# Kernel tuning notes

Measured on AMD Instinct MI355X. Metric: run time of the kernel, lower is better.

Reference implementation:

```python
import jax, jax.numpy as jnp
import numpy as np

D_MODEL = 1024
HEADS = 16
SEQ = 2048
BATCH = 4
NEG_INF = -1e9
LN_EPS = 1e-5


def setup_inputs() -> dict:
    key = jax.random.key(0)
    ks = jax.random.split(key, 10)
    B, S, D = BATCH, SEQ, D_MODEL
    # xavier_uniform bound for square D x D linear
    bound = np.sqrt(6.0 / (D + D))
    def xavier(k):
        return jax.random.uniform(k, (D, D), jnp.float32, -bound, bound)
    return {
        "q": jax.random.normal(ks[0], (B, S, D), jnp.float32),
        "k": jax.random.normal(ks[1], (B, S, D), jnp.float32),
        "v": jax.random.normal(ks[2], (B, S, D), jnp.float32),
        "Wq": xavier(ks[3]),
        "Wk": xavier(ks[4]),
        "Wv": xavier(ks[5]),
        "Wo": xavier(ks[6]),
        "ln_gamma": jnp.ones((D,), jnp.float32),
        "ln_beta": jnp.zeros((D,), jnp.float32),
        "sen_len": jax.random.randint(ks[7], (B,), 1, S + 1, jnp.int32),
    }


def reference(q, k, v, Wq, Wk, Wv, Wo, ln_gamma, ln_beta, sen_len):
    B, S, D = q.shape
    H = HEADS
    d = D // H
    residual = q
    # projections (Linear with weight W applies x @ W.T)
    qh = jnp.einsum('bsd,ed->bse', q, Wq).reshape(B, S, H, d).transpose(0, 2, 1, 3)
    kh = jnp.einsum('bsd,ed->bse', k, Wk).reshape(B, S, H, d).transpose(0, 2, 1, 3)
    vh = jnp.einsum('bsd,ed->bse', v, Wv).reshape(B, S, H, d).transpose(0, 2, 1, 3)
    # scores [B,H,S,S]
    scores = jnp.einsum('bhqd,bhkd->bhqk', qh, kh) / np.sqrt(d).astype(np.float32)
    # padding mask on keys: j >= sen_len[b]; causal mask: j > i
    pad = jnp.arange(S)[None, :] >= sen_len[:, None]          # [B, S]
    causal = jnp.triu(jnp.ones((S, S), bool), 1)               # [S, S]
    mask = pad[:, None, None, :] | causal[None, None, :, :]
    scores = jnp.where(mask, NEG_INF, scores)
    att = jax.nn.softmax(scores, axis=-1)
    ctx = jnp.einsum('bhqk,bhkd->bhqd', att, vh)               # [B,H,S,d]
    ctx = ctx.transpose(0, 2, 1, 3).reshape(B, S, D)
    out = jnp.einsum('bsd,ed->bse', ctx, Wo)
    out = out + residual
    mean = out.mean(-1, keepdims=True)
    var = out.var(-1, keepdims=True)
    out = (out - mean) * jax.lax.rsqrt(var + LN_EPS) * ln_gamma + ln_beta
    return out
```

## Files before the change

### kernel.cpp

```cpp
#include <hip/hip_runtime.h>

typedef __bf16 bf16;
typedef bf16 bf16x8 __attribute__((ext_vector_type(8)));
typedef bf16 bf16x4 __attribute__((ext_vector_type(4)));
typedef float f32x4 __attribute__((ext_vector_type(4)));

#define ASYNC16(gp, lp) __builtin_amdgcn_global_load_lds( \
    (__attribute__((address_space(1))) void*)(const void*)(gp), \
    (__attribute__((address_space(3))) void*)(lp), 16, 0, 0)

__device__ __forceinline__ bf16x8 cvt2(const float4 a, const float4 b) {
    bf16x8 t;
    t[0] = (bf16)a.x; t[1] = (bf16)a.y; t[2] = (bf16)a.z; t[3] = (bf16)a.w;
    t[4] = (bf16)b.x; t[5] = (bf16)b.y; t[6] = (bf16)b.z; t[7] = (bf16)b.w;
    return t;
}

__global__ __launch_bounds__(256)
void cvt_w3(const float* __restrict__ W0, const float* __restrict__ W1,
            const float* __restrict__ W2, bf16* __restrict__ out)
{
    const int z = blockIdx.y;
    const float* src = (z == 0) ? W0 : (z == 1) ? W1 : W2;
    const int i = blockIdx.x * 256 + threadIdx.x;
    const float4 a = ((const float4*)src)[i * 2];
    const float4 b = ((const float4*)src)[i * 2 + 1];
    *(bf16x8*)&out[((size_t)z << 20) + (size_t)i * 8] = cvt2(a, b);
}

__global__ __launch_bounds__(256)
void cvt_w1(const float* __restrict__ W, bf16* __restrict__ out)
{
    const int i = blockIdx.x * 256 + threadIdx.x;
    const float4 a = ((const float4*)W)[i * 2];
    const float4 b = ((const float4*)W)[i * 2 + 1];
    *(bf16x8*)&out[(size_t)i * 8] = cvt2(a, b);
}

__global__ __launch_bounds__(256, 2)
void proj_gemm(const float* __restrict__ Aq, const float* __restrict__ Ak,
               const float* __restrict__ Av, const bf16* __restrict__ Wb3,
               bf16* __restrict__ Qp, bf16* __restrict__ Kp, bf16* __restrict__ Vt)
{
    constexpr int K = 1024;
    constexpr int BK = 32;
    __shared__ __align__(16) bf16 As[128 * BK];
    __shared__ __align__(16) bf16 Bs[128 * BK];

    const int z = blockIdx.z;
    const float* A = (z == 0) ? Aq : (z == 1) ? Ak : Av;
    const bf16* W = Wb3 + ((size_t)z << 20);

    const int tid  = threadIdx.x;
    const int lane = tid & 63;
    const int w    = tid >> 6;
    const int wr   = w >> 1, wc = w & 1;
    const int m0   = blockIdx.y * 128;
    const int n0   = blockIdx.x * 128;

    f32x4 acc[4][4] = {};

    for (int k0 = 0; k0 < K; k0 += BK) {
        #pragma unroll
        for (int i = 0; i < 2; ++i) {
            const int c   = w * 128 + i * 64 + lane;
            const int row = c >> 2, kg = c & 3;
            ASYNC16(W + (size_t)(n0 + row) * K + k0 + kg * 8, &Bs[c * 8]);
            const float* ap = A + (size_t)(m0 + row) * K + k0 + kg * 8;
            *(bf16x8*)&As[c * 8] = cvt2(*(const float4*)ap, *(const float4*)(ap + 4));
        }
        __syncthreads();
        bf16x8 af[4], bfr[4];
        #pragma unroll
        for (int t = 0; t < 4; ++t) {
            af[t]  = *(const bf16x8*)&As[(wr * 64 + t * 16 + (lane & 15)) * BK + (lane >> 4) * 8];
            bfr[t] = *(const bf16x8*)&Bs[(wc * 64 + t * 16 + (lane & 15)) * BK + (lane >> 4) * 8];
        }
        #pragma unroll
        for (int mt = 0; mt < 4; ++mt)
            #pragma unroll
            for (int nt = 0; nt < 4; ++nt)
                acc[mt][nt] = __builtin_amdgcn_mfma_f32_16x16x32_bf16(af[mt], bfr[nt], acc[mt][nt], 0, 0, 0);
        __syncthreads();
    }

    #pragma unroll
    for (int mt = 0; mt < 4; ++mt) {
        #pragma unroll
        for (int nt = 0; nt < 4; ++nt) {
            const int mbase = m0 + wr * 64 + mt * 16 + ((lane >> 4) << 2);
            const int n     = n0 + wc * 64 + nt * 16 + (lane & 15);
            const int h = n >> 6, dd = n & 63;
            if (z < 2) {
                bf16* out = (z == 0) ? Qp : Kp;
                #pragma unroll
                for (int r = 0; r < 4; ++r) {
                    const int m = mbase + r;
                    const int b = m >> 11, s = m & 2047;
                    out[(((size_t)(b * 16 + h)) * 2048 + s) * 64 + dd] = (bf16)acc[mt][nt][r];
                }
            } else {
                const int b = mbase >> 11, s = mbase & 2047;
                bf16x4 v4;
                #pragma unroll
                for (int r = 0; r < 4; ++r) v4[r] = (bf16)acc[mt][nt][r];
                *(bf16x4*)&Vt[(((size_t)(b * 16 + h)) * 64 + dd) * 2048 + s] = v4;
            }
        }
    }
}

__global__ __launch_bounds__(256, 2)
void gemm_out(const bf16* __restrict__ A, const bf16* __restrict__ W,
              const float* __restrict__ R, float* __restrict__ out)
{
    constexpr int K = 1024;
    constexpr int BK = 32;
    __shared__ __align__(16) bf16 As[128 * BK];
    __shared__ __align__(16) bf16 Bs[128 * BK];

    const int tid  = threadIdx.x;
    const int lane = tid & 63;
    const int w    = tid >> 6;
    const int wr   = w >> 1, wc = w & 1;
    const int m0   = blockIdx.y * 128;
    const int n0   = blockIdx.x * 128;

    f32x4 acc[4][4] = {};

    for (int k0 = 0; k0 < K; k0 += BK) {
        #pragma unroll
        for (int i = 0; i < 2; ++i) {
            const int c   = w * 128 + i * 64 + lane;
            const int row = c >> 2, kg = c & 3;
            ASYNC16(A + (size_t)(m0 + row) * K + k0 + kg * 8, &As[c * 8]);
            ASYNC16(W + (size_t)(n0 + row) * K + k0 + kg * 8, &Bs[c * 8]);
        }
        __syncthreads();
        bf16x8 af[4], bfr[4];
        #pragma unroll
        for (int t = 0; t < 4; ++t) {
            af[t]  = *(const bf16x8*)&As[(wr * 64 + t * 16 + (lane & 15)) * BK + (lane >> 4) * 8];
            bfr[t] = *(const bf16x8*)&Bs[(wc * 64 + t * 16 + (lane & 15)) * BK + (lane >> 4) * 8];
        }
        #pragma unroll
        for (int mt = 0; mt < 4; ++mt)
            #pragma unroll
            for (int nt = 0; nt < 4; ++nt)
                acc[mt][nt] = __builtin_amdgcn_mfma_f32_16x16x32_bf16(af[mt], bfr[nt], acc[mt][nt], 0, 0, 0);
        __syncthreads();
    }

    #pragma unroll
    for (int mt = 0; mt < 4; ++mt) {
        #pragma unroll
        for (int nt = 0; nt < 4; ++nt) {
            const int mbase = m0 + wr * 64 + mt * 16 + ((lane >> 4) << 2);
            const int n     = n0 + wc * 64 + nt * 16 + (lane & 15);
            #pragma unroll
            for (int r = 0; r < 4; ++r) {
                const size_t idx = (size_t)(mbase + r) * 1024 + n;
                out[idx] = acc[mt][nt][r] + R[idx];
            }
        }
    }
}

__global__ __launch_bounds__(256, 2)
void attn_kernel(const bf16* __restrict__ Qp, const bf16* __restrict__ Kp,
                 const bf16* __restrict__ Vt, const int* __restrict__ sen_len,
                 bf16* __restrict__ ctx)
{
    const int qt = gridDim.x - 1 - blockIdx.x;
    const int h = blockIdx.y, b = blockIdx.z;
    const int q0 = qt * 128;
    const int bh = b * 16 + h;
    const int slen = sen_len[b];
    const int tid = threadIdx.x, lane = tid & 63, w = tid >> 6;
    const int wr = w >> 1, wc = w & 1;
    const float SCALE = 0.125f;
    const float SHIFT = 20.0f;

    __shared__ __align__(16) bf16 Ps[128 * 136];
    __shared__ float psum[2][128];

    bf16x8 qf[4][2];
    const bf16* Qbase = Qp + ((size_t)bh * 2048 + q0) * 64;
    #pragma unroll
    for (int mt = 0; mt < 4; ++mt)
        #pragma unroll
        for (int kk = 0; kk < 2; ++kk)
            qf[mt][kk] = *(const bf16x8*)(Qbase + (wr * 64 + mt * 16 + (lane & 15)) * 64
                                          + kk * 32 + (lane >> 4) * 8);

    f32x4 o[4][2] = {};
    float lsum[4][4] = {};

    const int jlim = min(q0 + 128, slen);
    const int nkt  = (jlim + 127) >> 7;

    const bf16* Kbh = Kp + (size_t)bh * 2048 * 64;
    const bf16* Vbh = Vt + (size_t)bh * 64 * 2048;

    for (int kt = 0; kt < nkt; ++kt) {
        const int k0 = kt * 128;

        f32x4 sf[4][4] = {};
        #pragma unroll
        for (int kk = 0; kk < 2; ++kk) {
            bf16x8 bk[4];
            #pragma unroll
            for (int nt = 0; nt < 4; ++nt)
                bk[nt] = *(const bf16x8*)(Kbh + (size_t)(k0 + wc * 64 + nt * 16 + (lane & 15)) * 64
                                          + kk * 32 + (lane >> 4) * 8);
            #pragma unroll
            for (int mt = 0; mt < 4; ++mt)
                #pragma unroll
                for (int nt = 0; nt < 4; ++nt)
                    sf[mt][nt] = __builtin_amdgcn_mfma_f32_16x16x32_bf16(qf[mt][kk], bk[nt], sf[mt][nt], 0, 0, 0);
        }

        if (kt == nkt - 1) {
            #pragma unroll
            for (int mt = 0; mt < 4; ++mt)
                #pragma unroll
                for (int r = 0; r < 4; ++r) {
                    const int row = wr * 64 + mt * 16 + ((lane >> 4) << 2) + r;
                    const int ig = q0 + row;
                    #pragma unroll
                    for (int nt = 0; nt < 4; ++nt) {
                        const int jg = k0 + wc * 64 + nt * 16 + (lane & 15);
                        const float sv = (jg > ig || jg >= slen) ? -1.0e9f : sf[mt][nt][r];
                        const float p = __expf(fmaf(sv, SCALE, -SHIFT));
                        lsum[mt][r] += p;
                        Ps[row * 136 + wc * 64 + nt * 16 + (lane & 15)] = (bf16)p;
                    }
                }
        } else {
            #pragma unroll
            for (int mt = 0; mt < 4; ++mt)
                #pragma unroll
                for (int r = 0; r < 4; ++r) {
                    const int row = wr * 64 + mt * 16 + ((lane >> 4) << 2) + r;
                    #pragma unroll
                    for (int nt = 0; nt < 4; ++nt) {
                        const float p = __expf(fmaf(sf[mt][nt][r], SCALE, -SHIFT));
                        lsum[mt][r] += p;
                        Ps[row * 136 + wc * 64 + nt * 16 + (lane & 15)] = (bf16)p;
                    }
                }
        }
        __syncthreads();

        #pragma unroll
        for (int ks = 0; ks < 4; ++ks) {
            bf16x8 pf[4], vf[2];
            #pragma unroll
            for (int mt = 0; mt < 4; ++mt)
                pf[mt] = *(const bf16x8*)&Ps[(wr * 64 + mt * 16 + (lane & 15)) * 136
                                             + ks * 32 + (lane >> 4) * 8];
            #pragma unroll
            for (int nt = 0; nt < 2; ++nt)
                vf[nt] = *(const bf16x8*)(Vbh + (size_t)(wc * 32 + nt * 16 + (lane & 15)) * 2048
                                          + k0 + ks * 32 + (lane >> 4) * 8);
            #pragma unroll
            for (int mt = 0; mt < 4; ++mt)
                #pragma unroll
                for (int nt = 0; nt < 2; ++nt)
                    o[mt][nt] = __builtin_amdgcn_mfma_f32_16x16x32_bf16(pf[mt], vf[nt], o[mt][nt], 0, 0, 0);
        }
        __syncthreads();
    }

    #pragma unroll
    for (int off = 1; off < 16; off <<= 1)
        #pragma unroll
        for (int mt = 0; mt < 4; ++mt)
            #pragma unroll
            for (int r = 0; r < 4; ++r)
                lsum[mt][r] += __shfl_xor(lsum[mt][r], off, 64);
    if ((lane & 15) == 0)
        #pragma unroll
        for (int mt = 0; mt < 4; ++mt)
            #pragma unroll
            for (int r = 0; r < 4; ++r)
                psum[wc][wr * 64 + mt * 16 + ((lane >> 4) << 2) + r] = lsum[mt][r];
    __syncthreads();

    #pragma unroll
    for (int mt = 0; mt < 4; ++mt)
        #pragma unroll
        for (int r = 0; r < 4; ++r) {
            const int row = wr * 64 + mt * 16 + ((lane >> 4) << 2) + r;
            const float inv = 1.0f / (psum[0][row] + psum[1][row]);
            const int sg = q0 + row;
            #pragma unroll
            for (int nt = 0; nt < 2; ++nt) {
                const int dd = wc * 32 + nt * 16 + (lane & 15);
                ctx[((size_t)(b * 2048 + sg)) * 1024 + h * 64 + dd] = (bf16)(o[mt][nt][r] * inv);
            }
        }
}

__global__ __launch_bounds__(256)
void ln_kernel(const float* __restrict__ y, const float* __restrict__ gamma,
               const float* __restrict__ beta, float* __restrict__ out)
{
    const int row = blockIdx.x;
    const int tid = threadIdx.x;
    const float4 v = ((const float4*)(y + (size_t)row * 1024))[tid];
    float s  = v.x + v.y + v.z + v.w;
    float s2 = v.x * v.x + v.y * v.y + v.z * v.z + v.w * v.w;
    #pragma unroll
    for (int o = 32; o > 0; o >>= 1) {
        s  += __shfl_down(s, o, 64);
        s2 += __shfl_down(s2, o, 64);
    }
    __shared__ float ps[4], ps2[4], stat[2];
    const int w = tid >> 6, lane = tid & 63;
    if (lane == 0) { ps[w] = s; ps2[w] = s2; }
    __syncthreads();
    if (tid == 0) {
        const float S  = ps[0] + ps[1] + ps[2] + ps[3];
        const float S2 = ps2[0] + ps2[1] + ps2[2] + ps2[3];
        const float mean = S * (1.0f / 1024.0f);
        const float var  = S2 * (1.0f / 1024.0f) - mean * mean;
        stat[0] = mean;
        stat[1] = rsqrtf(var + 1e-5f);
    }
    __syncthreads();
    const float mean = stat[0], rstd = stat[1];
    const float4 g4 = ((const float4*)gamma)[tid];
    const float4 b4 = ((const float4*)beta)[tid];
    float4 ov;
    ov.x = (v.x - mean) * rstd * g4.x + b4.x;
    ov.y = (v.y - mean) * rstd * g4.y + b4.y;
    ov.z = (v.z - mean) * rstd * g4.z + b4.z;
    ov.w = (v.w - mean) * rstd * g4.w + b4.w;
    ((float4*)(out + (size_t)row * 1024))[tid] = ov;
}

extern "C" void kernel_launch(void* const* d_in, const int* in_sizes, int n_in,
                              void* d_out, int out_size, void* d_ws, size_t ws_size,
                              hipStream_t stream)
{
    const float* q     = (const float*)d_in[0];
    const float* k     = (const float*)d_in[1];
    const float* v     = (const float*)d_in[2];
    const float* Wq    = (const float*)d_in[3];
    const float* Wk    = (const float*)d_in[4];
    const float* Wv    = (const float*)d_in[5];
    const float* Wo    = (const float*)d_in[6];
    const float* gamma = (const float*)d_in[7];
    const float* beta  = (const float*)d_in[8];
    const int*   sen   = (const int*)d_in[9];

    char* ws = (char*)d_ws;
    const size_t SEG = 16777216;
    bf16* Wb3 = (bf16*)ws;
    bf16* ctx = (bf16*)ws;
    bf16* Qp  = (bf16*)(ws + SEG);
    bf16* Kp  = (bf16*)(ws + 2 * SEG);
    bf16* Vt  = (bf16*)(ws + 3 * SEG);
    bf16* WoB = (bf16*)(ws + 3 * SEG);
    float* y  = (float*)(ws + SEG);

    dim3 bb(256);
    cvt_w3<<<dim3(512, 3), bb, 0, stream>>>(Wq, Wk, Wv, Wb3);
    proj_gemm<<<dim3(8, 64, 3), bb, 0, stream>>>(q, k, v, Wb3, Qp, Kp, Vt);
    attn_kernel<<<dim3(16, 16, 4), bb, 0, stream>>>(Qp, Kp, Vt, sen, ctx);
    cvt_w1<<<dim3(512), bb, 0, stream>>>(Wo, WoB);
    gemm_out<<<dim3(8, 64), bb, 0, stream>>>(ctx, WoB, q, y);
    ln_kernel<<<dim3(8192), bb, 0, stream>>>(y, gamma, beta, (float*)d_out);
}
```

Measured before the change: 351.8 us.

## Pre-convert q and k activations to bf16 and remap GEMM block order

Adds two conversion passes that turn q and k into bf16 copies held in the output buffer, so the projection GEMM can stream those A tiles with async global-to-LDS loads instead of converting fp32 in registers on every tile. V keeps the inline conversion path. Both GEMMs also remap block indices so consecutive blocks walk down M while sharing one N column, which aims for better weight-tile L2 reuse. Workspace buffers are reshuffled to fit. The trade-off is extra full passes over q and k, plus reliance on the output buffer as scratch.

```diff
diff --git a/kernel.cpp b/kernel.cpp
--- a/kernel.cpp
+++ b/kernel.cpp
@@ -14,6 +14,15 @@
     t[0] = (bf16)a.x; t[1] = (bf16)a.y; t[2] = (bf16)a.z; t[3] = (bf16)a.w;
     t[4] = (bf16)b.x; t[5] = (bf16)b.y; t[6] = (bf16)b.z; t[7] = (bf16)b.w;
     return t;
+}
+
+__global__ __launch_bounds__(256)
+void cvt_w1(const float* __restrict__ W, bf16* __restrict__ out)
+{
+    const int i = blockIdx.x * 256 + threadIdx.x;
+    const float4 a = ((const float4*)W)[i * 2];
+    const float4 b = ((const float4*)W)[i * 2 + 1];
+    *(bf16x8*)&out[(size_t)i * 8] = cvt2(a, b);
 }
 
 __global__ __launch_bounds__(256)
@@ -28,17 +37,8 @@
     *(bf16x8*)&out[((size_t)z << 20) + (size_t)i * 8] = cvt2(a, b);
 }
 
-__global__ __launch_bounds__(256)
-void cvt_w1(const float* __restrict__ W, bf16* __restrict__ out)
-{
-    const int i = blockIdx.x * 256 + threadIdx.x;
-    const float4 a = ((const float4*)W)[i * 2];
-    const float4 b = ((const float4*)W)[i * 2 + 1];
-    *(bf16x8*)&out[(size_t)i * 8] = cvt2(a, b);
-}
-
 __global__ __launch_bounds__(256, 2)
-void proj_gemm(const float* __restrict__ Aq, const float* __restrict__ Ak,
+void proj_gemm(const bf16* __restrict__ qb, const bf16* __restrict__ kb,
                const float* __restrict__ Av, const bf16* __restrict__ Wb3,
                bf16* __restrict__ Qp, bf16* __restrict__ Kp, bf16* __restrict__ Vt)
 {
@@ -48,15 +48,17 @@
     __shared__ __align__(16) bf16 Bs[128 * BK];
 
     const int z = blockIdx.z;
-    const float* A = (z == 0) ? Aq : (z == 1) ? Ak : Av;
     const bf16* W = Wb3 + ((size_t)z << 20);
 
     const int tid  = threadIdx.x;
     const int lane = tid & 63;
     const int w    = tid >> 6;
     const int wr   = w >> 1, wc = w & 1;
-    const int m0   = blockIdx.y * 128;
-    const int n0   = blockIdx.x * 128;
+    const int flat = blockIdx.y * 8 + blockIdx.x;
+    const int m0   = (flat & 63) * 128;
+    const int n0   = (flat >> 6) * 128;
+
+    const bf16* Ab = (z == 0) ? qb : kb;
 
     f32x4 acc[4][4] = {};
 
@@ -66,8 +68,12 @@
             const int c   = w * 128 + i * 64 + lane;
             const int row = c >> 2, kg = c & 3;
             ASYNC16(W + (size_t)(n0 + row) * K + k0 + kg * 8, &Bs[c * 8]);
-            const float* ap = A + (size_t)(m0 + row) * K + k0 + kg * 8;
-            *(bf16x8*)&As[c * 8] = cvt2(*(const float4*)ap, *(const float4*)(ap + 4));
+            if (z < 2) {
+                ASYNC16(Ab + (size_t)(m0 + row) * K + k0 + kg * 8, &As[c * 8]);
+            } else {
+                const float* ap = Av + (size_t)(m0 + row) * K + k0 + kg * 8;
+                *(bf16x8*)&As[c * 8] = cvt2(*(const float4*)ap, *(const float4*)(ap + 4));
+            }
         }
         __syncthreads();
         bf16x8 af[4], bfr[4];
@@ -123,8 +129,9 @@
     const int lane = tid & 63;
     const int w    = tid >> 6;
     const int wr   = w >> 1, wc = w & 1;
-    const int m0   = blockIdx.y * 128;
-    const int n0   = blockIdx.x * 128;
+    const int flat = blockIdx.y * 8 + blockIdx.x;
+    const int m0   = (flat & 63) * 128;
+    const int n0   = (flat >> 6) * 128;
 
     f32x4 acc[4][4] = {};
 
@@ -356,18 +363,23 @@
     const int*   sen   = (const int*)d_in[9];
 
     char* ws = (char*)d_ws;
+    char* ob = (char*)d_out;
     const size_t SEG = 16777216;
-    bf16* Wb3 = (bf16*)ws;
-    bf16* ctx = (bf16*)ws;
-    bf16* Qp  = (bf16*)(ws + SEG);
-    bf16* Kp  = (bf16*)(ws + 2 * SEG);
-    bf16* Vt  = (bf16*)(ws + 3 * SEG);
+    bf16* qb  = (bf16*)ob;
+    bf16* kb  = (bf16*)(ob + SEG);
+    bf16* ctx = (bf16*)ob;
+    bf16* Qp  = (bf16*)(ws);
+    bf16* Kp  = (bf16*)(ws + SEG);
+    bf16* Vt  = (bf16*)(ws + 2 * SEG);
+    bf16* Wb3 = (bf16*)(ws + 3 * SEG);
     bf16* WoB = (bf16*)(ws + 3 * SEG);
-    float* y  = (float*)(ws + SEG);
+    float* y  = (float*)ws;
 
     dim3 bb(256);
+    cvt_w1<<<dim3(4096), bb, 0, stream>>>(q, qb);
+    cvt_w1<<<dim3(4096), bb, 0, stream>>>(k, kb);
     cvt_w3<<<dim3(512, 3), bb, 0, stream>>>(Wq, Wk, Wv, Wb3);
-    proj_gemm<<<dim3(8, 64, 3), bb, 0, stream>>>(q, k, v, Wb3, Qp, Kp, Vt);
+    proj_gemm<<<dim3(8, 64, 3), bb, 0, stream>>>(qb, kb, v, Wb3, Qp, Kp, Vt);
     attn_kernel<<<dim3(16, 16, 4), bb, 0, stream>>>(Qp, Kp, Vt, sen, ctx);
     cvt_w1<<<dim3(512), bb, 0, stream>>>(Wo, WoB);
     gemm_out<<<dim3(8, 64), bb, 0, stream>>>(ctx, WoB, q, y);
```

New measurement: 352.6 us. No clear change (+0.2%).
